# Optimization experiments

Measured on AMD Instinct MI355X. Metric: run time of the kernel, lower is better.

## Reference

```python
import jax, jax.numpy as jnp
import numpy as np

SEQ_LEN, BATCH, INPUT_SIZE, HIDDEN = 2048, 64, 256, 512


def setup_inputs() -> dict:
    key = jax.random.key(0)
    ks = jax.random.split(key, 6)
    s_i = 1.0 / np.sqrt(HIDDEN)
    return {
        "x": jax.random.normal(ks[0], (SEQ_LEN, BATCH, INPUT_SIZE), dtype=jnp.float32),
        "keep_mask": jax.random.randint(ks[1], (HIDDEN,), 0, 2, dtype=jnp.int32),
        # PyTorch nn.LSTM params, gate order (i, f, g, o) stacked on dim 0
        "W_ih": jax.random.uniform(ks[2], (4 * HIDDEN, INPUT_SIZE), jnp.float32, -s_i, s_i),
        "W_hh": jax.random.uniform(ks[3], (4 * HIDDEN, HIDDEN), jnp.float32, -s_i, s_i),
        "b_ih": jax.random.uniform(ks[4], (4 * HIDDEN,), jnp.float32, -s_i, s_i),
        "b_hh": jax.random.uniform(ks[5], (4 * HIDDEN,), jnp.float32, -s_i, s_i),
    }


def _masked_lstm(x, keep_mask, W_ih, W_hh, b_ih, b_hh):
    H = W_hh.shape[1]
    keep = keep_mask.astype(bool)  # [H]; h channels where keep==False are zeroed each step
    # precompute input contribution for all timesteps: [T, B, 4H]
    x_gates = jnp.einsum("tbi,gi->tbg", x, W_ih) + b_ih + b_hh

    def step(carry, xg_t):
        h, c = carry  # [B, H] each
        gates = xg_t + h @ W_hh.T  # [B, 4H]
        i, f, g, o = jnp.split(gates, 4, axis=-1)
        c = jax.nn.sigmoid(f) * c + jax.nn.sigmoid(i) * jnp.tanh(g)
        h = jax.nn.sigmoid(o) * jnp.tanh(c)
        h = jnp.where(keep, h, 0.0)  # mask applied to h BEFORE it feeds next step
        return (h, c), h

    B = x.shape[1]
    h0 = jnp.zeros((B, H), x.dtype)
    c0 = jnp.zeros((B, H), x.dtype)
    (h_t, c_t), output = jax.lax.scan(step, (h0, c0), x_gates)
    return output, h_t, c_t


def reference(x, keep_mask, W_ih, W_hh, b_ih, b_hh):
    output, h_t, c_t = _masked_lstm(x, keep_mask, W_ih, W_hh, b_ih, b_hh)
    # match torch module: (output [T,B,H], (h_n [1,B,H], c_n [1,B,H]))
    return output, (h_t[None], c_t[None])
```

## Files before the change

kernel.cpp:

```cpp
#include <hip/hip_runtime.h>

#define T_STEPS 2048
#define NBATCH  64
#define ISZ     256
#define HID     512
#define BH      (NBATCH*HID)

typedef __attribute__((ext_vector_type(8))) __bf16 bf16x8;
typedef __attribute__((ext_vector_type(4))) float  f32x4;
typedef __attribute__((ext_vector_type(4))) unsigned int u32x4;

#define MFMA __builtin_amdgcn_mfma_f32_16x16x32_bf16

__device__ __forceinline__ float sigm(float v){ return 1.0f/(1.0f+expf(-v)); }

__device__ __forceinline__ unsigned int pack2(__bf16 a, __bf16 b){
    return (unsigned int)__builtin_bit_cast(unsigned short,a)
         | ((unsigned int)__builtin_bit_cast(unsigned short,b)<<16);
}

__global__ void __launch_bounds__(256,1)
lstm_persist(const float* __restrict__ x, const int* __restrict__ keep,
             const float* __restrict__ Wih, const float* __restrict__ Whh,
             const float* __restrict__ bih, const float* __restrict__ bhh,
             float* __restrict__ outp, unsigned long long* __restrict__ exch)
{
    __shared__ float G[4][8][32];
    __shared__ float C[8][32];
    __shared__ __align__(16) char XB[2][8][1024];
    __shared__ __align__(16) char HXs[8][1024];

    const int tid=threadIdx.x, wv=tid>>6, lane=tid&63, bid=blockIdx.x;
    const int g=bid&7, w=bid>>3, ch0=w*32, bbase=g*8;
    const int n=lane&15, lg=lane>>4, nr=(n<8)?n:7;


    bf16x8 whh0[2][16], whh1[2][16], wih0[2][8], wih1[2][8];
    float biasv[2];
#pragma unroll
    for (int nt=0; nt<2; ++nt){
        const int row = wv*HID + ch0 + nt*16 + n;
        const float* wr = Whh + (size_t)row*HID + lg*8;
#pragma unroll
        for (int kt=0; kt<16; ++kt){
            const float* p = wr + kt*32;
            bf16x8 b0,b1;
#pragma unroll
            for(int e=0;e<8;++e){
                float f=p[e]; __bf16 hh=(__bf16)f;
                b0[e]=hh; b1[e]=(__bf16)(f-(float)hh);
            }
            whh0[nt][kt]=b0; whh1[nt][kt]=b1;
        }
        const float* wr2 = Wih + (size_t)row*ISZ + lg*8;
#pragma unroll
        for (int kt=0; kt<8; ++kt){
            const float* p = wr2 + kt*32;
            bf16x8 b0,b1;
#pragma unroll
            for(int e=0;e<8;++e){
                float f=p[e]; __bf16 hh=(__bf16)f;
                b0[e]=hh; b1[e]=(__bf16)(f-(float)hh);
            }
            wih0[nt][kt]=b0; wih1[nt][kt]=b1;
        }
        biasv[nt] = bih[row] + bhh[row];
    }

    const int erow = tid>>5, ech = tid&31;
    const int kp = keep[ch0 + ech];
    C[erow][ech] = 0.0f;

    const int c64 = tid&63, row0 = tid>>6, row1 = row0+4;

    {
        const char* s0 = (const char*)x + ((size_t)(bbase+row0)*ISZ)*4 + (size_t)c64*16;
        const char* s1 = (const char*)x + ((size_t)(bbase+row1)*ISZ)*4 + (size_t)c64*16;
        u32x4 q0 = *(const u32x4*)s0, q1 = *(const u32x4*)s1;
        *(u32x4*)&XB[0][row0][(c64^row0)*16] = q0;
        *(u32x4*)&XB[0][row1][(c64^row1)*16] = q1;
    }
    __syncthreads();

    for (int t=0; t<T_STEPS; ++t){
        const bool hasx = (t+1<T_STEPS);
        u32x4 xq0, xq1;
        if (hasx){
            const char* s0 = (const char*)x + (((size_t)(t+1)*NBATCH + bbase+row0)*ISZ)*4 + (size_t)c64*16;
            const char* s1 = (const char*)x + (((size_t)(t+1)*NBATCH + bbase+row1)*ISZ)*4 + (size_t)c64*16;
            xq0 = *(const u32x4*)s0;
            xq1 = *(const u32x4*)s1;
        }

        f32x4 a0v[2] = {{biasv[0],biasv[0],biasv[0],biasv[0]},
                        {biasv[1],biasv[1],biasv[1],biasv[1]}};
        f32x4 a1v[2] = {{0,0,0,0},{0,0,0,0}};
#pragma unroll
        for (int kt2=0; kt2<8; ++kt2){
            f32x4 xa = *(const f32x4*)&XB[t&1][nr][(((kt2*8)+lg*2+0)^nr)*16];
            f32x4 xb = *(const f32x4*)&XB[t&1][nr][(((kt2*8)+lg*2+1)^nr)*16];
            bf16x8 a0,a1;
#pragma unroll
            for(int e=0;e<4;++e){
                float f=xa[e]; __bf16 hh=(__bf16)f;
                a0[e]=hh; a1[e]=(__bf16)(f-(float)hh);
                f=xb[e]; hh=(__bf16)f;
                a0[e+4]=hh; a1[e+4]=(__bf16)(f-(float)hh);
            }
            a0v[0]=MFMA(a0,wih0[0][kt2],a0v[0],0,0,0);
            a0v[1]=MFMA(a0,wih0[1][kt2],a0v[1],0,0,0);
            a1v[0]=MFMA(a0,wih1[0][kt2],a1v[0],0,0,0);
            a1v[1]=MFMA(a0,wih1[1][kt2],a1v[1],0,0,0);
            a1v[0]=MFMA(a1,wih0[0][kt2],a1v[0],0,0,0);
            a1v[1]=MFMA(a1,wih0[1][kt2],a1v[1],0,0,0);
        }

        u32x4 hq0, hq1;
        if (t>0){
            const unsigned int need = (unsigned int)t;
            const unsigned long long* e64 = exch + (size_t)(g*2 + ((t-1)&1))*2048;
            unsigned long long q[8];
            while(1){
#pragma unroll
                for (int j=0;j<4;++j)
                    q[j]   = __hip_atomic_load(e64 + (size_t)tid*4 + j,
                                               __ATOMIC_RELAXED, __HIP_MEMORY_SCOPE_AGENT);
#pragma unroll
                for (int j=0;j<4;++j)
                    q[4+j] = __hip_atomic_load(e64 + (size_t)(tid+256)*4 + j,
                                               __ATOMIC_RELAXED, __HIP_MEMORY_SCOPE_AGENT);
                bool ok = true;
#pragma unroll
                for (int j=0;j<8;++j) ok &= ((unsigned int)(q[j]>>32) == need);
                if (ok) break;
                __builtin_amdgcn_s_sleep(1);
            }
            hq0[0]=(unsigned int)q[0]; hq0[1]=(unsigned int)q[1];
            hq0[2]=(unsigned int)q[2]; hq0[3]=(unsigned int)q[3];
            hq1[0]=(unsigned int)q[4]; hq1[1]=(unsigned int)q[5];
            hq1[2]=(unsigned int)q[6]; hq1[3]=(unsigned int)q[7];
        }

        if (t>0){
            *(u32x4*)&HXs[row0][(c64^row0)*16] = hq0;
            *(u32x4*)&HXs[row1][(c64^row1)*16] = hq1;
        }
        if (hasx){
            *(u32x4*)&XB[(t+1)&1][row0][(c64^row0)*16] = xq0;
            *(u32x4*)&XB[(t+1)&1][row1][(c64^row1)*16] = xq1;
        }
        __syncthreads();

        if (t>0){
#pragma unroll
            for (int kt=0;kt<16;++kt){
                bf16x8 h0 = *(const bf16x8*)&HXs[nr][(((kt*4)+lg)^nr)*16];
                a0v[0]=MFMA(h0,whh0[0][kt],a0v[0],0,0,0);
                a0v[1]=MFMA(h0,whh0[1][kt],a0v[1],0,0,0);
                a1v[0]=MFMA(h0,whh1[0][kt],a1v[0],0,0,0);
                a1v[1]=MFMA(h0,whh1[1][kt],a1v[1],0,0,0);
            }
        }

        if (lane<32){
#pragma unroll
            for (int nt=0; nt<2; ++nt){
                f32x4 acc = a0v[nt]+a1v[nt];
#pragma unroll
                for(int r=0;r<4;++r) G[wv][lg*4+r][nt*16+n]=acc[r];
            }
        }
        __syncthreads();

        float gi=G[0][erow][ech], gf=G[1][erow][ech], gg=G[2][erow][ech], go=G[3][erow][ech];
        float cc = sigm(gf)*C[erow][ech] + sigm(gi)*tanhf(gg);
        C[erow][ech]=cc;
        float hh = sigm(go)*tanhf(cc); if(!kp) hh=0.0f;

        float hnb = __shfl_xor(hh, 1);
        if (!(tid&1)){
            unsigned long long val = ((unsigned long long)(unsigned int)(t+1) << 32)
                                   | (unsigned long long)pack2((__bf16)hh, (__bf16)hnb);
            __hip_atomic_store(exch + (size_t)(g*2+(t&1))*2048 + erow*256 + ((ch0+ech)>>1),
                               val, __ATOMIC_RELAXED, __HIP_MEMORY_SCOPE_AGENT);
        }

        outp[(size_t)t*BH + (size_t)(bbase+erow)*HID + ch0+ech] = hh;
        if (t==T_STEPS-1){
            outp[(size_t)T_STEPS*BH + (size_t)(bbase+erow)*HID + ch0+ech]      = hh;
            outp[(size_t)T_STEPS*BH + BH + (size_t)(bbase+erow)*HID + ch0+ech] = cc;
        }
    }
}

extern "C" void kernel_launch(void* const* d_in, const int* in_sizes, int n_in,
                              void* d_out, int out_size, void* d_ws, size_t ws_size,
                              hipStream_t stream)
{
    const void *px = nullptr, *pk = nullptr, *pwi = nullptr, *pwh = nullptr,
               *pb0 = nullptr, *pb1 = nullptr;
    for (int i = 0; i < n_in; ++i) {
        const long s = (long)in_sizes[i];
        if      (s == (long)T_STEPS * NBATCH * ISZ) px  = d_in[i];
        else if (s == HID)                          pk  = d_in[i];
        else if (s == 4L * HID * ISZ)               pwi = d_in[i];
        else if (s == 4L * HID * HID)               pwh = d_in[i];
        else if (s == 4L * HID) { if (!pb0) pb0 = d_in[i]; else pb1 = d_in[i]; }
    }
    if (!px || !pk || !pwi || !pwh || !pb0 || !pb1) {
        px = d_in[0]; pk = d_in[1]; pwi = d_in[2]; pwh = d_in[3]; pb0 = d_in[4]; pb1 = d_in[5];
    }

    lstm_persist<<<dim3(128), dim3(256), 0, stream>>>(
        (const float*)px, (const int*)pk, (const float*)pwi, (const float*)pwh,
        (const float*)pb0, (const float*)pb1, (float*)d_out,
        (unsigned long long*)d_ws);
}
```

Measured before the change: 6.689 ms.

## Process 16 batch rows per block with 64 blocks and hoisted exchange polling

Each block now handles 16 batch rows instead of 8, which fills all 16 MFMA rows that were previously half wasted, and the grid shrinks from 128 to 64 persistent blocks. With four batch groups instead of eight, each exchange group has 16 participants per group rather than 16 per smaller group, and the total number of blocks that must synchronise each step is halved. The first poll of the h exchange is issued before the x-projection MFMAs so its latency overlaps compute. The cell state moves from shared memory into registers, with two channels per thread and vectorised output stores. The cost is twice the MFMA work per block on the critical path and half as many CUs in use.

```diff
diff --git a/kernel.cpp b/kernel.cpp
--- a/kernel.cpp
+++ b/kernel.cpp
@@ -8,6 +8,7 @@
 
 typedef __attribute__((ext_vector_type(8))) __bf16 bf16x8;
 typedef __attribute__((ext_vector_type(4))) float  f32x4;
+typedef __attribute__((ext_vector_type(2))) float  f32x2;
 typedef __attribute__((ext_vector_type(4))) unsigned int u32x4;
 
 #define MFMA __builtin_amdgcn_mfma_f32_16x16x32_bf16
@@ -25,14 +26,13 @@
              const float* __restrict__ bih, const float* __restrict__ bhh,
              float* __restrict__ outp, unsigned long long* __restrict__ exch)
 {
-    __shared__ float G[4][8][32];
-    __shared__ float C[8][32];
-    __shared__ __align__(16) char XB[2][8][1024];
-    __shared__ __align__(16) char HXs[8][1024];
+    __shared__ float G[4][16][32];
+    __shared__ __align__(16) char XB[2][16][1024];
+    __shared__ __align__(16) char HXs[16][1024];
 
     const int tid=threadIdx.x, wv=tid>>6, lane=tid&63, bid=blockIdx.x;
-    const int g=bid&7, w=bid>>3, ch0=w*32, bbase=g*8;
-    const int n=lane&15, lg=lane>>4, nr=(n<8)?n:7;
+    const int g=bid&3, w=bid>>2, ch0=w*32, bbase=g*16;
+    const int n=lane&15, lg=lane>>4;
 
 
     bf16x8 whh0[2][16], whh1[2][16], wih0[2][8], wih1[2][8];
@@ -67,29 +67,43 @@
         biasv[nt] = bih[row] + bhh[row];
     }
 
-    const int erow = tid>>5, ech = tid&31;
-    const int kp = keep[ch0 + ech];
-    C[erow][ech] = 0.0f;
-
-    const int c64 = tid&63, row0 = tid>>6, row1 = row0+4;
-
-    {
-        const char* s0 = (const char*)x + ((size_t)(bbase+row0)*ISZ)*4 + (size_t)c64*16;
-        const char* s1 = (const char*)x + ((size_t)(bbase+row1)*ISZ)*4 + (size_t)c64*16;
-        u32x4 q0 = *(const u32x4*)s0, q1 = *(const u32x4*)s1;
-        *(u32x4*)&XB[0][row0][(c64^row0)*16] = q0;
-        *(u32x4*)&XB[0][row1][(c64^row1)*16] = q1;
+    const int erow = tid>>4, epair=(tid&15)*2;
+    const int kp0 = keep[ch0+epair], kp1 = keep[ch0+epair+1];
+    float c0v = 0.0f, c1v = 0.0f;
+
+    const int c64 = tid&63;
+
+#pragma unroll
+    for (int j=0;j<4;++j){
+        const int r = wv + j*4;
+        u32x4 q = *(const u32x4*)((const char*)x + ((size_t)(bbase+r)*ISZ)*4 + (size_t)c64*16);
+        *(u32x4*)&XB[0][r][(c64^r)*16] = q;
     }
     __syncthreads();
 
     for (int t=0; t<T_STEPS; ++t){
         const bool hasx = (t+1<T_STEPS);
-        u32x4 xq0, xq1;
+        u32x4 xq[4];
         if (hasx){
-            const char* s0 = (const char*)x + (((size_t)(t+1)*NBATCH + bbase+row0)*ISZ)*4 + (size_t)c64*16;
-            const char* s1 = (const char*)x + (((size_t)(t+1)*NBATCH + bbase+row1)*ISZ)*4 + (size_t)c64*16;
-            xq0 = *(const u32x4*)s0;
-            xq1 = *(const u32x4*)s1;
+#pragma unroll
+            for (int j=0;j<4;++j){
+                const int r = wv + j*4;
+                xq[j] = *(const u32x4*)((const char*)x
+                        + (((size_t)(t+1)*NBATCH + bbase+r)*ISZ)*4 + (size_t)c64*16);
+            }
+        }
+
+        unsigned long long q64[16];
+        const unsigned long long* e64 = exch + (size_t)(g*2 + ((t-1)&1))*4096;
+        if (t>0){
+#pragma unroll
+            for (int j=0;j<4;++j){
+                const int r = wv + j*4;
+#pragma unroll
+                for (int jj=0;jj<4;++jj)
+                    q64[j*4+jj] = __hip_atomic_load(e64 + (size_t)r*256 + c64*4 + jj,
+                                                    __ATOMIC_RELAXED, __HIP_MEMORY_SCOPE_AGENT);
+            }
         }
 
         f32x4 a0v[2] = {{biasv[0],biasv[0],biasv[0],biasv[0]},
@@ -97,8 +111,8 @@
         f32x4 a1v[2] = {{0,0,0,0},{0,0,0,0}};
 #pragma unroll
         for (int kt2=0; kt2<8; ++kt2){
-            f32x4 xa = *(const f32x4*)&XB[t&1][nr][(((kt2*8)+lg*2+0)^nr)*16];
-            f32x4 xb = *(const f32x4*)&XB[t&1][nr][(((kt2*8)+lg*2+1)^nr)*16];
+            f32x4 xa = *(const f32x4*)&XB[t&1][n][(((kt2*8)+lg*2+0)^n)*16];
+            f32x4 xb = *(const f32x4*)&XB[t&1][n][(((kt2*8)+lg*2+1)^n)*16];
             bf16x8 a0,a1;
 #pragma unroll
             for(int e=0;e<4;++e){
@@ -115,46 +129,51 @@
             a1v[1]=MFMA(a1,wih0[1][kt2],a1v[1],0,0,0);
         }
 
-        u32x4 hq0, hq1;
+        u32x4 hq[4];
         if (t>0){
             const unsigned int need = (unsigned int)t;
-            const unsigned long long* e64 = exch + (size_t)(g*2 + ((t-1)&1))*2048;
-            unsigned long long q[8];
             while(1){
-#pragma unroll
-                for (int j=0;j<4;++j)
-                    q[j]   = __hip_atomic_load(e64 + (size_t)tid*4 + j,
-                                               __ATOMIC_RELAXED, __HIP_MEMORY_SCOPE_AGENT);
-#pragma unroll
-                for (int j=0;j<4;++j)
-                    q[4+j] = __hip_atomic_load(e64 + (size_t)(tid+256)*4 + j,
-                                               __ATOMIC_RELAXED, __HIP_MEMORY_SCOPE_AGENT);
                 bool ok = true;
 #pragma unroll
-                for (int j=0;j<8;++j) ok &= ((unsigned int)(q[j]>>32) == need);
+                for (int j=0;j<16;++j) ok &= ((unsigned int)(q64[j]>>32) == need);
                 if (ok) break;
                 __builtin_amdgcn_s_sleep(1);
-            }
-            hq0[0]=(unsigned int)q[0]; hq0[1]=(unsigned int)q[1];
-            hq0[2]=(unsigned int)q[2]; hq0[3]=(unsigned int)q[3];
-            hq1[0]=(unsigned int)q[4]; hq1[1]=(unsigned int)q[5];
-            hq1[2]=(unsigned int)q[6]; hq1[3]=(unsigned int)q[7];
-        }
-
-        if (t>0){
-            *(u32x4*)&HXs[row0][(c64^row0)*16] = hq0;
-            *(u32x4*)&HXs[row1][(c64^row1)*16] = hq1;
+#pragma unroll
+                for (int j=0;j<4;++j){
+                    const int r = wv + j*4;
+#pragma unroll
+                    for (int jj=0;jj<4;++jj)
+                        q64[j*4+jj] = __hip_atomic_load(e64 + (size_t)r*256 + c64*4 + jj,
+                                                        __ATOMIC_RELAXED, __HIP_MEMORY_SCOPE_AGENT);
+                }
+            }
+#pragma unroll
+            for (int j=0;j<4;++j){
+                hq[j][0]=(unsigned int)q64[j*4+0]; hq[j][1]=(unsigned int)q64[j*4+1];
+                hq[j][2]=(unsigned int)q64[j*4+2]; hq[j][3]=(unsigned int)q64[j*4+3];
+            }
+        }
+
+        if (t>0){
+#pragma unroll
+            for (int j=0;j<4;++j){
+                const int r = wv + j*4;
+                *(u32x4*)&HXs[r][(c64^r)*16] = hq[j];
+            }
         }
         if (hasx){
-            *(u32x4*)&XB[(t+1)&1][row0][(c64^row0)*16] = xq0;
-            *(u32x4*)&XB[(t+1)&1][row1][(c64^row1)*16] = xq1;
+#pragma unroll
+            for (int j=0;j<4;++j){
+                const int r = wv + j*4;
+                *(u32x4*)&XB[(t+1)&1][r][(c64^r)*16] = xq[j];
+            }
         }
         __syncthreads();
 
         if (t>0){
 #pragma unroll
             for (int kt=0;kt<16;++kt){
-                bf16x8 h0 = *(const bf16x8*)&HXs[nr][(((kt*4)+lg)^nr)*16];
+                bf16x8 h0 = *(const bf16x8*)&HXs[n][(((kt*4)+lg)^n)*16];
                 a0v[0]=MFMA(h0,whh0[0][kt],a0v[0],0,0,0);
                 a0v[1]=MFMA(h0,whh0[1][kt],a0v[1],0,0,0);
                 a1v[0]=MFMA(h0,whh1[0][kt],a1v[0],0,0,0);
@@ -162,33 +181,37 @@
             }
         }
 
-        if (lane<32){
-#pragma unroll
-            for (int nt=0; nt<2; ++nt){
-                f32x4 acc = a0v[nt]+a1v[nt];
-#pragma unroll
-                for(int r=0;r<4;++r) G[wv][lg*4+r][nt*16+n]=acc[r];
-            }
+#pragma unroll
+        for (int nt=0; nt<2; ++nt){
+            f32x4 acc = a0v[nt]+a1v[nt];
+#pragma unroll
+            for(int r=0;r<4;++r) G[wv][lg*4+r][nt*16+n]=acc[r];
         }
         __syncthreads();
 
-        float gi=G[0][erow][ech], gf=G[1][erow][ech], gg=G[2][erow][ech], go=G[3][erow][ech];
-        float cc = sigm(gf)*C[erow][ech] + sigm(gi)*tanhf(gg);
-        C[erow][ech]=cc;
-        float hh = sigm(go)*tanhf(cc); if(!kp) hh=0.0f;
-
-        float hnb = __shfl_xor(hh, 1);
-        if (!(tid&1)){
+        f32x2 gi = *(const f32x2*)&G[0][erow][epair];
+        f32x2 gf = *(const f32x2*)&G[1][erow][epair];
+        f32x2 gg = *(const f32x2*)&G[2][erow][epair];
+        f32x2 go = *(const f32x2*)&G[3][erow][epair];
+        c0v = sigm(gf[0])*c0v + sigm(gi[0])*tanhf(gg[0]);
+        c1v = sigm(gf[1])*c1v + sigm(gi[1])*tanhf(gg[1]);
+        float h0f = sigm(go[0])*tanhf(c0v); if(!kp0) h0f=0.0f;
+        float h1f = sigm(go[1])*tanhf(c1v); if(!kp1) h1f=0.0f;
+
+        {
             unsigned long long val = ((unsigned long long)(unsigned int)(t+1) << 32)
-                                   | (unsigned long long)pack2((__bf16)hh, (__bf16)hnb);
-            __hip_atomic_store(exch + (size_t)(g*2+(t&1))*2048 + erow*256 + ((ch0+ech)>>1),
+                                   | (unsigned long long)pack2((__bf16)h0f,(__bf16)h1f);
+            __hip_atomic_store(exch + (size_t)(g*2+(t&1))*4096
+                                    + (size_t)erow*256 + ((ch0+epair)>>1),
                                val, __ATOMIC_RELAXED, __HIP_MEMORY_SCOPE_AGENT);
         }
 
-        outp[(size_t)t*BH + (size_t)(bbase+erow)*HID + ch0+ech] = hh;
+        f32x2 ov; ov[0]=h0f; ov[1]=h1f;
+        *(f32x2*)(outp + (size_t)t*BH + (size_t)(bbase+erow)*HID + ch0+epair) = ov;
         if (t==T_STEPS-1){
-            outp[(size_t)T_STEPS*BH + (size_t)(bbase+erow)*HID + ch0+ech]      = hh;
-            outp[(size_t)T_STEPS*BH + BH + (size_t)(bbase+erow)*HID + ch0+ech] = cc;
+            f32x2 cv; cv[0]=c0v; cv[1]=c1v;
+            *(f32x2*)(outp + (size_t)T_STEPS*BH + (size_t)(bbase+erow)*HID + ch0+epair)      = ov;
+            *(f32x2*)(outp + (size_t)T_STEPS*BH + BH + (size_t)(bbase+erow)*HID + ch0+epair) = cv;
         }
     }
 }
@@ -211,7 +234,7 @@
         px = d_in[0]; pk = d_in[1]; pwi = d_in[2]; pwh = d_in[3]; pb0 = d_in[4]; pb1 = d_in[5];
     }
 
-    lstm_persist<<<dim3(128), dim3(256), 0, stream>>>(
+    lstm_persist<<<dim3(64), dim3(256), 0, stream>>>(
         (const float*)px, (const int*)pk, (const float*)pwi, (const float*)pwh,
         (const float*)pb0, (const float*)pb1, (float*)d_out,
         (unsigned long long*)d_ws);
```

Result: slower. 10.53 ms (+57.4%).

## Remap gate rows per wave so LSTM cell update stays in registers

Applied to the files above, without the earlier changes.

Reorders the weight rows each wave holds so that all four gates for a channel sit in one wave's MFMA accumulators, with i/f and g/o paired across lane halves. The cell update now runs in registers via lane shuffles, with the cell state kept in registers, which removes the shared-memory gate exchange and one block barrier per timestep. The h staging buffer is double-buffered so the remaining barrier can cover both phases. Only a quarter of lanes do the elementwise work, and the output and exchange stores become vectorised float2 writes.

```diff
diff --git a/kernel.cpp b/kernel.cpp
--- a/kernel.cpp
+++ b/kernel.cpp
@@ -8,6 +8,7 @@
 
 typedef __attribute__((ext_vector_type(8))) __bf16 bf16x8;
 typedef __attribute__((ext_vector_type(4))) float  f32x4;
+typedef __attribute__((ext_vector_type(2))) float  f32x2;
 typedef __attribute__((ext_vector_type(4))) unsigned int u32x4;
 
 #define MFMA __builtin_amdgcn_mfma_f32_16x16x32_bf16
@@ -25,10 +26,8 @@
              const float* __restrict__ bih, const float* __restrict__ bhh,
              float* __restrict__ outp, unsigned long long* __restrict__ exch)
 {
-    __shared__ float G[4][8][32];
-    __shared__ float C[8][32];
     __shared__ __align__(16) char XB[2][8][1024];
-    __shared__ __align__(16) char HXs[8][1024];
+    __shared__ __align__(16) char HXs[2][8][1024];
 
     const int tid=threadIdx.x, wv=tid>>6, lane=tid&63, bid=blockIdx.x;
     const int g=bid&7, w=bid>>3, ch0=w*32, bbase=g*8;
@@ -39,8 +38,9 @@
     float biasv[2];
 #pragma unroll
     for (int nt=0; nt<2; ++nt){
-        const int row = wv*HID + ch0 + nt*16 + n;
-        const float* wr = Whh + (size_t)row*HID + lg*8;
+        const int gsel = 2*nt + (n>>3);
+        const int wrow = gsel*HID + ch0 + wv*8 + (n&7);
+        const float* wr = Whh + (size_t)wrow*HID + lg*8;
 #pragma unroll
         for (int kt=0; kt<16; ++kt){
             const float* p = wr + kt*32;
@@ -52,7 +52,7 @@
             }
             whh0[nt][kt]=b0; whh1[nt][kt]=b1;
         }
-        const float* wr2 = Wih + (size_t)row*ISZ + lg*8;
+        const float* wr2 = Wih + (size_t)wrow*ISZ + lg*8;
 #pragma unroll
         for (int kt=0; kt<8; ++kt){
             const float* p = wr2 + kt*32;
@@ -64,19 +64,19 @@
             }
             wih0[nt][kt]=b0; wih1[nt][kt]=b1;
         }
-        biasv[nt] = bih[row] + bhh[row];
-    }
-
-    const int erow = tid>>5, ech = tid&31;
-    const int kp = keep[ch0 + ech];
-    C[erow][ech] = 0.0f;
+        biasv[nt] = bih[wrow] + bhh[wrow];
+    }
+
+    const int  cN = ch0 + wv*8 + n;
+    const bool ew = (lg<2) && (n<8);
+    int kp = 1; if (ew) kp = keep[cN];
+    float creg[4] = {0.f,0.f,0.f,0.f};
 
     const int c64 = tid&63, row0 = tid>>6, row1 = row0+4;
 
     {
-        const char* s0 = (const char*)x + ((size_t)(bbase+row0)*ISZ)*4 + (size_t)c64*16;
-        const char* s1 = (const char*)x + ((size_t)(bbase+row1)*ISZ)*4 + (size_t)c64*16;
-        u32x4 q0 = *(const u32x4*)s0, q1 = *(const u32x4*)s1;
+        u32x4 q0 = *(const u32x4*)((const char*)x + ((size_t)(bbase+row0)*ISZ)*4 + (size_t)c64*16);
+        u32x4 q1 = *(const u32x4*)((const char*)x + ((size_t)(bbase+row1)*ISZ)*4 + (size_t)c64*16);
         *(u32x4*)&XB[0][row0][(c64^row0)*16] = q0;
         *(u32x4*)&XB[0][row1][(c64^row1)*16] = q1;
     }
@@ -86,10 +86,8 @@
         const bool hasx = (t+1<T_STEPS);
         u32x4 xq0, xq1;
         if (hasx){
-            const char* s0 = (const char*)x + (((size_t)(t+1)*NBATCH + bbase+row0)*ISZ)*4 + (size_t)c64*16;
-            const char* s1 = (const char*)x + (((size_t)(t+1)*NBATCH + bbase+row1)*ISZ)*4 + (size_t)c64*16;
-            xq0 = *(const u32x4*)s0;
-            xq1 = *(const u32x4*)s1;
+            xq0 = *(const u32x4*)((const char*)x + (((size_t)(t+1)*NBATCH + bbase+row0)*ISZ)*4 + (size_t)c64*16);
+            xq1 = *(const u32x4*)((const char*)x + (((size_t)(t+1)*NBATCH + bbase+row1)*ISZ)*4 + (size_t)c64*16);
         }
 
         f32x4 a0v[2] = {{biasv[0],biasv[0],biasv[0],biasv[0]},
@@ -142,8 +140,8 @@
         }
 
         if (t>0){
-            *(u32x4*)&HXs[row0][(c64^row0)*16] = hq0;
-            *(u32x4*)&HXs[row1][(c64^row1)*16] = hq1;
+            *(u32x4*)&HXs[t&1][row0][(c64^row0)*16] = hq0;
+            *(u32x4*)&HXs[t&1][row1][(c64^row1)*16] = hq1;
         }
         if (hasx){
             *(u32x4*)&XB[(t+1)&1][row0][(c64^row0)*16] = xq0;
@@ -154,7 +152,7 @@
         if (t>0){
 #pragma unroll
             for (int kt=0;kt<16;++kt){
-                bf16x8 h0 = *(const bf16x8*)&HXs[nr][(((kt*4)+lg)^nr)*16];
+                bf16x8 h0 = *(const bf16x8*)&HXs[t&1][nr][(((kt*4)+lg)^nr)*16];
                 a0v[0]=MFMA(h0,whh0[0][kt],a0v[0],0,0,0);
                 a0v[1]=MFMA(h0,whh0[1][kt],a0v[1],0,0,0);
                 a1v[0]=MFMA(h0,whh1[0][kt],a1v[0],0,0,0);
@@ -162,33 +160,52 @@
             }
         }
 
-        if (lane<32){
-#pragma unroll
-            for (int nt=0; nt<2; ++nt){
-                f32x4 acc = a0v[nt]+a1v[nt];
-#pragma unroll
-                for(int r=0;r<4;++r) G[wv][lg*4+r][nt*16+n]=acc[r];
-            }
-        }
-        __syncthreads();
-
-        float gi=G[0][erow][ech], gf=G[1][erow][ech], gg=G[2][erow][ech], go=G[3][erow][ech];
-        float cc = sigm(gf)*C[erow][ech] + sigm(gi)*tanhf(gg);
-        C[erow][ech]=cc;
-        float hh = sigm(go)*tanhf(cc); if(!kp) hh=0.0f;
-
-        float hnb = __shfl_xor(hh, 1);
-        if (!(tid&1)){
-            unsigned long long val = ((unsigned long long)(unsigned int)(t+1) << 32)
-                                   | (unsigned long long)pack2((__bf16)hh, (__bf16)hnb);
-            __hip_atomic_store(exch + (size_t)(g*2+(t&1))*2048 + erow*256 + ((ch0+ech)>>1),
-                               val, __ATOMIC_RELAXED, __HIP_MEMORY_SCOPE_AGENT);
-        }
-
-        outp[(size_t)t*BH + (size_t)(bbase+erow)*HID + ch0+ech] = hh;
+        f32x4 aS0 = a0v[0]+a1v[0];
+        f32x4 aS1 = a0v[1]+a1v[1];
+        float hv[4] = {0.f,0.f,0.f,0.f};
+#pragma unroll
+        for (int r=0;r<4;++r){
+            float fo = __shfl_xor(aS0[r], 8);
+            float oo = __shfl_xor(aS1[r], 8);
+            if (ew){
+                creg[r] = sigm(fo)*creg[r] + sigm(aS0[r])*tanhf(aS1[r]);
+                float hh = sigm(oo)*tanhf(creg[r]); if(!kp) hh=0.0f;
+                hv[r] = hh;
+            }
+        }
+
+        float hn0 = __shfl_xor(hv[0],1), hn1 = __shfl_xor(hv[1],1);
+        float hn2 = __shfl_xor(hv[2],1), hn3 = __shfl_xor(hv[3],1);
+        if (ew && !(n&1)){
+            const float hn[4] = {hn0,hn1,hn2,hn3};
+            unsigned long long* eb = exch + (size_t)(g*2+(t&1))*2048 + (cN>>1);
+#pragma unroll
+            for (int r=0;r<4;++r){
+                unsigned long long val = ((unsigned long long)(unsigned int)(t+1) << 32)
+                                       | (unsigned long long)pack2((__bf16)hv[r],(__bf16)hn[r]);
+                __hip_atomic_store(eb + (size_t)(lg*4+r)*256, val,
+                                   __ATOMIC_RELAXED, __HIP_MEMORY_SCOPE_AGENT);
+            }
+#pragma unroll
+            for (int r=0;r<4;++r){
+                f32x2 ov; ov[0]=hv[r]; ov[1]=hn[r];
+                *(f32x2*)(outp + (size_t)t*BH + (size_t)(bbase+lg*4+r)*HID + cN) = ov;
+            }
+        }
         if (t==T_STEPS-1){
-            outp[(size_t)T_STEPS*BH + (size_t)(bbase+erow)*HID + ch0+ech]      = hh;
-            outp[(size_t)T_STEPS*BH + BH + (size_t)(bbase+erow)*HID + ch0+ech] = cc;
+            float cn0=__shfl_xor(creg[0],1), cn1=__shfl_xor(creg[1],1);
+            float cn2=__shfl_xor(creg[2],1), cn3=__shfl_xor(creg[3],1);
+            if (ew && !(n&1)){
+                const float hn[4] = {hn0,hn1,hn2,hn3};
+                const float cn[4] = {cn0,cn1,cn2,cn3};
+#pragma unroll
+                for (int r=0;r<4;++r){
+                    f32x2 hvv; hvv[0]=hv[r];   hvv[1]=hn[r];
+                    f32x2 cvv; cvv[0]=creg[r]; cvv[1]=cn[r];
+                    *(f32x2*)(outp + (size_t)T_STEPS*BH + (size_t)(bbase+lg*4+r)*HID + cN)      = hvv;
+                    *(f32x2*)(outp + (size_t)T_STEPS*BH + BH + (size_t)(bbase+lg*4+r)*HID + cN) = cvv;
+                }
+            }
         }
     }
 }
```

New measurement: 9.690 ms. 1.45x slower.
